# Kernel tuning notes

Hardware: AMD Instinct MI355X
Metric: run time of the kernel (lower is better)

Reference implementation:

```python
import jax, jax.numpy as jnp
import numpy as np

EPS = float(np.finfo(float).eps)
NUM_RFS = 1

def conv3d(x, w):
    # x: [N,C,D,H,W], w: [O,I,kd,kh,kw], VALID, stride 1 (matches F.conv3d defaults)
    return jax.lax.conv_general_dilated(
        x, w, window_strides=(1, 1, 1), padding='VALID',
        dimension_numbers=('NCDHW', 'OIDHW', 'NCDHW'))

def setup_inputs() -> dict:
    key = jax.random.key(0)
    k1, k2, k3, k4 = jax.random.split(key, 4)
    x = jax.random.normal(k1, (1, 1, 3, 394, 394), jnp.float32)
    x_prev = jax.random.normal(k2, (1, 1, 3, 394, 394), jnp.float32)
    # params stored post-permute as [out_ch, in_ch, kt, kh, kw]
    filts_temp = jax.random.normal(k3, (16, 1, 3, 11, 11), jnp.float32)
    filts_notemp = jax.random.normal(k4, (16, 1, 1, 11, 11), jnp.float32)
    return {"x": x, "x_prev": x_prev, "filts_temp": filts_temp, "filts_notemp": filts_notemp}

def reference(x, x_prev, filts_temp, filts_notemp):
    corr_x = NUM_RFS * filts_temp.shape[3]  # kh
    corr_y = NUM_RFS * filts_temp.shape[4]  # kw
    num_filts = filts_temp.shape[0] + filts_notemp.shape[0]

    def feats(v):
        vt = jax.nn.relu(conv3d(v, filts_temp)) / 2           # [1,16,1,H',W'] (T==kt)
        vn = jax.nn.relu(conv3d(v[:, :, -1:, :, :], filts_notemp))  # last frame, [1,16,1,H',W']
        return jnp.concatenate([vt, vn], axis=1)              # [1,32,1,H',W']

    f = feats(x)
    fp = feats(x_prev)
    # channel-wise normalization
    x1 = f / (jnp.sum(f, axis=1, keepdims=True) + EPS)
    x1_prev = fp / (jnp.sum(fp, axis=1, keepdims=True) + EPS)

    y_max, x_max = x1.shape[3], x1.shape[4]
    yc = y_max - 2 * corr_y
    xc = x_max - 2 * corr_x
    # cropped current-frame channels become conv filters: [nf,1,1,yc,xc]
    x1_filts = x1[:, :, :, corr_y:y_max - corr_y, corr_x:x_max - corr_x].reshape(
        num_filts, 1, 1, yc, xc)
    prev = x1_prev.reshape(1, 1, num_filts, y_max, x_max)
    # normalized cross-correlation via conv3d: out [1, nf, nf, 2cy+1, 2cx+1]
    x2 = conv3d(prev, x1_filts)
    x2 = x2.reshape(1, num_filts, num_filts, 2 * corr_y + 1, 2 * corr_x + 1)
    x2 = x2 / ((y_max - 2 * corr_y) * (x_max - 2 * corr_y))  # faithful to original (uses corr_y twice)
    return x1, x2
```

## Files before the change

### kernel.cpp

```cpp
#include <hip/hip_runtime.h>
#include <hip/hip_bf16.h>


typedef unsigned short ushort_t;
typedef unsigned int uint_t;
typedef unsigned char uchar_t;
typedef __attribute__((ext_vector_type(4))) float f32x4;
typedef __attribute__((ext_vector_type(16))) float f32x16;
typedef __attribute__((ext_vector_type(4))) uint_t uint4_t;
typedef __attribute__((ext_vector_type(2))) uint_t uint2_t;
typedef __attribute__((ext_vector_type(8))) int int8v;

#define EPSF 2.2204460492503131e-16f
#define X1_N (32*384*384)
#define X2_N (32*32*23*23)

#define FILTB_ROW_B 12288
#define FILTB_BYTES (372*48*32*8)
#define PREVB_STRIDE 432
#define PREVB_BYTES (32*385*PREVB_STRIDE)
#define ZERO_BYTES ((size_t)FILTB_BYTES + PREVB_BYTES)
#define FT2_ELEMS (16*45*12)

#define YMAX 367
#define NCHUNKS 16
#define INV_AREA (1.0f/131044.0f)

#define SB_COPY_B 432
#define SB_DYB_B  (8*SB_COPY_B)
#define SB_ROW_B  (4*SB_DYB_B)
#define SB_BYTES  (2*2*SB_ROW_B)

#define SA_BYTES  (8*FILTB_ROW_B)
#define SMEM_TOTAL (SA_BYTES + SB_BYTES)

__device__ __forceinline__ uint_t f32_to_e4m3(float f) {
  if (f < 0.015625f)
    return (uint_t)__float2int_rn(f * 512.0f);
  uint_t b = __builtin_bit_cast(uint_t, f);
  int e = (int)(b >> 23) - 127;
  uint_t m = b & 0x7FFFFFu;
  uint_t keep = m >> 20;
  uint_t rest = m & 0xFFFFFu;
  keep += (rest > 0x80000u) || (rest == 0x80000u && (keep & 1u));
  if (keep == 8u) { keep = 0u; e += 1; }
  if (e > 8) return 0x7Eu;
  return (uint_t)(((e + 7) << 3) | keep);
}

__global__ void prep_kernel(const float* __restrict__ ft, const float* __restrict__ fn,
                            float* __restrict__ fT2)
{
  const int e = blockIdx.x * 256 + threadIdx.x;
  if (e < FT2_ELEMS) {
    const int chp = e / 540;
    const int rem = e - chp * 540;
    const int row = rem / 12;
    const int j = rem - row * 12;
    float v = 0.f;
    if (j < 11) {
      if (row < 33)      v = ft[chp * 363 + row * 11 + j];
      else if (row < 44) v = fn[chp * 121 + (row - 33) * 11 + j];
    }
    fT2[e] = v;
  }
}

__global__ __launch_bounds__(128, 4) void feat_kernel(
    const float* __restrict__ xcur, const float* __restrict__ xprev,
    const float* __restrict__ fT2,
    float* __restrict__ out_x1, uchar_t* __restrict__ prevb)
{
  __shared__ float sPx[3 * 18 * 28];
  const int tid = threadIdx.x;
  const int chp = tid & 15;
  const int r = tid >> 4;
  const int j0 = blockIdx.x * 16;
  const int i0 = blockIdx.y * 8;
  const int i = i0 + r;
  const int mode = blockIdx.z;
  const float* __restrict__ xin = mode ? xprev : xcur;

  for (int e = tid; e < 3 * 18 * 26; e += 128) {
    const int t = e / 468;
    const int rem = e - t * 468;
    const int ri = rem / 26;
    const int ci = rem - ri * 26;
    sPx[(t * 18 + ri) * 28 + ci] = xin[((size_t)t * 394 + i0 + ri) * 394 + j0 + ci];
  }
  __syncthreads();

  const float* __restrict__ fbase = fT2 + chp * 540;

  float accT[16], accN[16];
#pragma unroll
  for (int p = 0; p < 16; ++p) { accT[p] = 0.f; accN[p] = 0.f; }

#pragma unroll
  for (int t = 0; t < 3; ++t) {
    for (int a = 0; a < 11; ++a) {
      const float* row = &sPx[(t * 18 + r + a) * 28];
      float wv[26];
#pragma unroll
      for (int k = 0; k < 6; ++k) {
        const f32x4 q = *(const f32x4*)(row + 4 * k);
        wv[4 * k + 0] = q[0]; wv[4 * k + 1] = q[1];
        wv[4 * k + 2] = q[2]; wv[4 * k + 3] = q[3];
      }
      wv[24] = row[24]; wv[25] = row[25];

      const float* fr = fbase + (t * 11 + a) * 12;
      const f32x4 fq0 = *(const f32x4*)(fr);
      const f32x4 fq1 = *(const f32x4*)(fr + 4);
      const f32x4 fq2 = *(const f32x4*)(fr + 8);
      float fv[12];
#pragma unroll
      for (int k = 0; k < 4; ++k) { fv[k] = fq0[k]; fv[4+k] = fq1[k]; fv[8+k] = fq2[k]; }
      float fv2[12];
      if (t == 2) {
        const float* fr2 = fbase + (33 + a) * 12;
        const f32x4 g0 = *(const f32x4*)(fr2);
        const f32x4 g1 = *(const f32x4*)(fr2 + 4);
        const f32x4 g2 = *(const f32x4*)(fr2 + 8);
#pragma unroll
        for (int k = 0; k < 4; ++k) { fv2[k] = g0[k]; fv2[4+k] = g1[k]; fv2[8+k] = g2[k]; }
      }

#pragma unroll
      for (int b = 0; b < 11; ++b) {
        const float fT = fv[b];
#pragma unroll
        for (int p = 0; p < 16; ++p) accT[p] = fmaf(wv[b + p], fT, accT[p]);
        if (t == 2) {
          const float fN = fv2[b];
#pragma unroll
          for (int p = 0; p < 16; ++p) accN[p] = fmaf(wv[b + p], fN, accN[p]);
        }
      }
    }
  }

  float o0[16], o1[16];
#pragma unroll
  for (int p = 0; p < 16; ++p) {
    const float vT = fmaxf(accT[p], 0.f) * 0.5f;
    const float vN = fmaxf(accN[p], 0.f);
    float s = vT + vN;
    s += __shfl_xor(s, 1);  s += __shfl_xor(s, 2);
    s += __shfl_xor(s, 4);  s += __shfl_xor(s, 8);
    const float inv = 1.f / (s + EPSF);
    o0[p] = vT * inv;
    o1[p] = vN * inv;
  }

  if (mode == 0) {
#pragma unroll
    for (int q = 0; q < 4; ++q) {
      f32x4 v0 = {o0[4*q], o0[4*q+1], o0[4*q+2], o0[4*q+3]};
      f32x4 v1 = {o1[4*q], o1[4*q+1], o1[4*q+2], o1[4*q+3]};
      *(f32x4*)(out_x1 + (size_t)chp * 147456 + i * 384 + j0 + 4 * q) = v0;
      *(f32x4*)(out_x1 + (size_t)(chp + 16) * 147456 + i * 384 + j0 + 4 * q) = v1;
    }
  } else {
    uint4_t u0, u1;
#pragma unroll
    for (int q = 0; q < 4; ++q) {
      u0[q] = f32_to_e4m3(o0[4*q]) | (f32_to_e4m3(o0[4*q+1]) << 8) |
              (f32_to_e4m3(o0[4*q+2]) << 16) | (f32_to_e4m3(o0[4*q+3]) << 24);
      u1[q] = f32_to_e4m3(o1[4*q]) | (f32_to_e4m3(o1[4*q+1]) << 8) |
              (f32_to_e4m3(o1[4*q+2]) << 16) | (f32_to_e4m3(o1[4*q+3]) << 24);
    }
    *(uint4_t*)(prevb + ((size_t)chp * 385 + i) * PREVB_STRIDE + j0) = u0;
    *(uint4_t*)(prevb + ((size_t)(chp + 16) * 385 + i) * PREVB_STRIDE + j0) = u1;
  }
}

__global__ __launch_bounds__(256) void pack_kernel(
    const float* __restrict__ x1, uchar_t* __restrict__ filtb)
{
  const int e = blockIdx.x * 256 + threadIdx.x;
  if (e >= 362 * 46 * 32) return;
  const int o = e & 31;
  const int q = e >> 5;
  const int xb = q % 46;
  const int rowr = q / 46 + 5;
  const int i = rowr + 6;
  const int j0 = 11 + xb * 8;
  const float* src = x1 + (size_t)o * 147456 + i * 384 + j0;
  uint_t w0 = 0, w1 = 0;
#pragma unroll
  for (int k = 0; k < 4; ++k) {
    w0 |= f32_to_e4m3((j0 + k     <= 372) ? src[k]     : 0.f) << (8 * k);
    w1 |= f32_to_e4m3((j0 + 4 + k <= 372) ? src[4 + k] : 0.f) << (8 * k);
  }
  uint2_t u = {w0, w1};
  const int off = (xb >> 3) * 2048 + ((xb >> 1) & 1) * 1024 +
                  ((xb >> 2) & 1) * 512 + o * 16 + (xb & 1) * 8;
  *(uint2_t*)(filtb + (size_t)rowr * FILTB_ROW_B + off) = u;
}

__global__ __launch_bounds__(768, 3) void corr_kernel(
    const uchar_t* __restrict__ filtb, const uchar_t* __restrict__ prevb,
    float* __restrict__ x2)
{
  extern __shared__ uchar_t smem[];

  const int tid = threadIdx.x;
  const int lane = tid & 63;
  const int wv = tid >> 6;
  const int cg = (wv >= 6) ? 1 : 0;
  const int w = wv - 6 * cg;
  const int kg = lane >> 5;
  const int nn = lane & 31;

  const int chpair = blockIdx.x / NCHUNKS;
  const int chunk = blockIdx.x % NCHUNKS;
  const int ch = 2 * chpair + cg;
  const int y0 = (chunk * YMAX) / NCHUNKS;
  const int y1 = ((chunk + 1) * YMAX) / NCHUNKS;

  uint_t* const sBg = (uint_t*)(smem + SA_BYTES) + cg * (2 * (SB_ROW_B / 4));

  int boffB[3];
#pragma unroll
  for (int nt = 0; nt < 3; ++nt) {
    const int n = nt * 32 + nn;
    const int dyb = n / 24;
    const int dxr = n - 24 * dyb;
    const int dx = (dxr < 23) ? dxr : 22;
    const int s = dx & 7;
    boffB[nt] = dyb * SB_DYB_B + s * SB_COPY_B + (dx >> 3) * 8 + kg * 32;
  }

  const int tl = tid - cg * 384;
  const bool st_act = (tl < 104);
  const int sdyb = st_act ? (tl / 26) : 0;
  const int sg = tl - 26 * (st_act ? (tl / 26) : 0);
  const uchar_t* srcbase = prevb + ((size_t)(ch * 385 + 6 * sdyb)) * PREVB_STRIDE;
  const int dstoff = sdyb * (SB_DYB_B / 4) + 4 * sg;

  uint_t st0 = 0, st1 = 0, st2 = 0, st3 = 0, st4 = 0, st5 = 0;

  auto load_st = [&](int yy) {
    const uint_t* sw = (const uint_t*)(srcbase + (size_t)yy * PREVB_STRIDE) + 4 * sg;
    const uint4_t lo = *(const uint4_t*)(sw);
    const uint2_t hi = *(const uint2_t*)(sw + 4);
    st0 = lo.x; st1 = lo.y; st2 = lo.z; st3 = lo.w; st4 = hi.x; st5 = hi.y;
  };

  auto write_shift = [&](int buf) {
    uint_t* dst = sBg + buf * (SB_ROW_B / 4) + dstoff;
    const uint_t wd[6] = {st0, st1, st2, st3, st4, st5};
#pragma unroll
    for (int s = 0; s < 8; ++s) {
      const int off = s >> 2;
      const int b = (s & 3) * 8;
      uint4_t v;
      if (b == 0) {
        v = uint4_t{wd[off], wd[off + 1], wd[off + 2], wd[off + 3]};
      } else {
        v = uint4_t{(wd[off]     >> b) | (wd[off + 1] << (32 - b)),
                    (wd[off + 1] >> b) | (wd[off + 2] << (32 - b)),
                    (wd[off + 2] >> b) | (wd[off + 3] << (32 - b)),
                    (wd[off + 3] >> b) | (wd[off + 4] << (32 - b))};
      }
      *(uint4_t*)(dst + s * (SB_COPY_B / 4)) = v;
    }
  };

  f32x16 acc[3];
#pragma unroll
  for (int nt = 0; nt < 3; ++nt)
#pragma unroll
    for (int r = 0; r < 16; ++r) acc[nt][r] = 0.f;

  {
    uint4_t pv[6];
#pragma unroll
    for (int r6 = 0; r6 < 6; ++r6)
      pv[r6] = *(const uint4_t*)(filtb + (size_t)(y0 + r6) * FILTB_ROW_B + tid * 16);
#pragma unroll
    for (int r6 = 0; r6 < 6; ++r6)
      *(uint4_t*)(smem + ((y0 + r6) & 7) * FILTB_ROW_B + tid * 16) = pv[r6];
  }
  if (st_act) {
    load_st(y0);
    write_shift(0);
    if (y0 + 1 < y1) load_st(y0 + 1);
  }

  __syncthreads();

  for (int y = y0; y < y1; ++y) {
    const int pb = (y - y0) & 1;

    const bool a_act = (y + 6 <= y1 + 4);
    uint4_t aval;
    if (a_act)
      aval = *(const uint4_t*)(filtb + (size_t)(y + 6) * FILTB_ROW_B + tid * 16);

    if (st_act && y + 1 < y1) write_shift(pb ^ 1);
    if (st_act && y + 2 < y1) load_st(y + 2);

    const char* sBrd = (const char*)sBg + pb * SB_ROW_B;
    const char* aRow = (const char*)smem +
        ((y + 5 - w) & 7) * FILTB_ROW_B + kg * 512 + nn * 16;

#pragma unroll 1
    for (int kt = 0; kt < 6; ++kt) {
      const char* ap = aRow + (kt << 11);
      const uint4_t a0 = *(const uint4_t*)(ap);
      const uint4_t a1 = *(const uint4_t*)(ap + 1024);
      const int8v Af = {(int)a0.x, (int)a0.y, (int)a0.z, (int)a0.w,
                        (int)a1.x, (int)a1.y, (int)a1.z, (int)a1.w};
#pragma unroll
      for (int nt = 0; nt < 3; ++nt) {
        const char* bp = sBrd + boffB[nt] + (kt << 6);
        const uint2_t b0 = *(const uint2_t*)(bp);
        const uint2_t b1 = *(const uint2_t*)(bp + 8);
        const uint2_t b2 = *(const uint2_t*)(bp + 16);
        const uint2_t b3 = *(const uint2_t*)(bp + 24);
        const int8v Bf = {(int)b0.x, (int)b0.y, (int)b1.x, (int)b1.y,
                          (int)b2.x, (int)b2.y, (int)b3.x, (int)b3.y};
        acc[nt] = __builtin_amdgcn_mfma_scale_f32_32x32x64_f8f6f4(
            Af, Bf, acc[nt], 0, 0,
            0, 0x7F7F7F7F, 0, 0x7F7F7F7F);
      }
    }

    if (a_act)
      *(uint4_t*)(smem + ((y + 6) & 7) * FILTB_ROW_B + tid * 16) = aval;

    __syncthreads();
  }

#pragma unroll
  for (int nt = 0; nt < 3; ++nt) {
    const int n = nt * 32 + nn;
    const int dyb = n / 24;
    const int dxr = n - 24 * dyb;
    if (dxr < 23) {
      const int dy = w + 6 * dyb;
      if (dy <= 22) {
#pragma unroll
        for (int r = 0; r < 16; ++r) {
          const int o = (r & 3) + 8 * (r >> 2) + 4 * kg;
          atomicAdd(&x2[((o * 32 + ch) * 23 + dy) * 23 + dxr],
                    acc[nt][r] * INV_AREA);
        }
      }
    }
  }
}

extern "C" void kernel_launch(void* const* d_in, const int* in_sizes, int n_in,
                              void* d_out, int out_size, void* d_ws, size_t ws_size,
                              hipStream_t stream)
{
  const float* x     = (const float*)d_in[0];
  const float* xprev = (const float*)d_in[1];
  const float* ft    = (const float*)d_in[2];
  const float* fn    = (const float*)d_in[3];
  float* out = (float*)d_out;

  uchar_t* filtb = (uchar_t*)d_ws;
  uchar_t* prevb = filtb + FILTB_BYTES;
  float* fT2 = (float*)(prevb + PREVB_BYTES);

  static bool attr_set = false;
  if (!attr_set) {
    (void)hipFuncSetAttribute((const void*)corr_kernel,
        hipFuncAttributeMaxDynamicSharedMemorySize, SMEM_TOTAL);
    attr_set = true;
  }

  hipMemsetAsync(d_ws, 0, ZERO_BYTES, stream);
  hipMemsetAsync(out + X1_N, 0, (size_t)X2_N * sizeof(float), stream);

  prep_kernel<<<dim3((FT2_ELEMS + 255) / 256), 256, 0, stream>>>(ft, fn, fT2);
  feat_kernel<<<dim3(24, 48, 2), 128, 0, stream>>>(x, xprev, fT2, out, prevb);
  pack_kernel<<<dim3((362 * 46 * 32 + 255) / 256), 256, 0, stream>>>(out, filtb);
  corr_kernel<<<dim3(16 * NCHUNKS), 768, SMEM_TOTAL, stream>>>(
      filtb, prevb, out + X1_N);
}
```

Measured before the change: 276.5 us.

## Software-pipeline MFMA operand loads, pad shared B rows, stage x1 stores via LDS

The correlation kernel's inner loop now prefetches the next A fragment and the next B fragment from shared memory while the current MFMA runs, so LDS latency overlaps matrix work. The per-dy block stride in the shared B buffer gets 16 bytes of padding, presumably to reduce bank conflicts. The feature kernel stages normalized x1 outputs through a shared tile so each thread writes contiguous 16-byte chunks in a coalesced pattern. In exchange there is extra register pressure from the double-buffered operands, more shared memory use, and an added barrier in the feature kernel.

Measured after the change: 278.9 us. Within noise of the previous version (+0.9%).

```diff
diff --git a/kernel.cpp b/kernel.cpp
--- a/kernel.cpp
+++ b/kernel.cpp
@@ -27,7 +27,7 @@
 #define INV_AREA (1.0f/131044.0f)
 
 #define SB_COPY_B 432
-#define SB_DYB_B  (8*SB_COPY_B)
+#define SB_DYB_B  (8*SB_COPY_B + 16)
 #define SB_ROW_B  (4*SB_DYB_B)
 #define SB_BYTES  (2*2*SB_ROW_B)
 
@@ -72,6 +72,7 @@
     float* __restrict__ out_x1, uchar_t* __restrict__ prevb)
 {
   __shared__ float sPx[3 * 18 * 28];
+  __shared__ float sOut[32][9][20];
   const int tid = threadIdx.x;
   const int chp = tid & 15;
   const int r = tid >> 4;
@@ -155,11 +156,20 @@
 
   if (mode == 0) {
 #pragma unroll
-    for (int q = 0; q < 4; ++q) {
-      f32x4 v0 = {o0[4*q], o0[4*q+1], o0[4*q+2], o0[4*q+3]};
-      f32x4 v1 = {o1[4*q], o1[4*q+1], o1[4*q+2], o1[4*q+3]};
-      *(f32x4*)(out_x1 + (size_t)chp * 147456 + i * 384 + j0 + 4 * q) = v0;
-      *(f32x4*)(out_x1 + (size_t)(chp + 16) * 147456 + i * 384 + j0 + 4 * q) = v1;
+    for (int p = 0; p < 16; ++p) {
+      sOut[chp][r][p] = o0[p];
+      sOut[chp + 16][r][p] = o1[p];
+    }
+    __syncthreads();
+#pragma unroll
+    for (int it = 0; it < 8; ++it) {
+      const int idx = it * 128 + tid;
+      const int seg = idx & 3;
+      const int rr = (idx >> 2) & 7;
+      const int chn = idx >> 5;
+      const f32x4 v = {sOut[chn][rr][4 * seg], sOut[chn][rr][4 * seg + 1],
+                       sOut[chn][rr][4 * seg + 2], sOut[chn][rr][4 * seg + 3]};
+      *(f32x4*)(out_x1 + (size_t)chn * 147456 + (i0 + rr) * 384 + j0 + 4 * seg) = v;
     }
   } else {
     uint4_t u0, u1;
@@ -306,26 +316,67 @@
     const char* aRow = (const char*)smem +
         ((y + 5 - w) & 7) * FILTB_ROW_B + kg * 512 + nn * 16;
 
+    int8v Af, Afn, Bf, Bfn;
+    {
+      const uint4_t a0 = *(const uint4_t*)(aRow);
+      const uint4_t a1 = *(const uint4_t*)(aRow + 1024);
+      Af = int8v{(int)a0.x, (int)a0.y, (int)a0.z, (int)a0.w,
+                 (int)a1.x, (int)a1.y, (int)a1.z, (int)a1.w};
+      const char* bp = sBrd + boffB[0];
+      const uint2_t b0 = *(const uint2_t*)(bp);
+      const uint2_t b1 = *(const uint2_t*)(bp + 8);
+      const uint2_t b2 = *(const uint2_t*)(bp + 16);
+      const uint2_t b3 = *(const uint2_t*)(bp + 24);
+      Bf = int8v{(int)b0.x, (int)b0.y, (int)b1.x, (int)b1.y,
+                 (int)b2.x, (int)b2.y, (int)b3.x, (int)b3.y};
+    }
 #pragma unroll 1
     for (int kt = 0; kt < 6; ++kt) {
-      const char* ap = aRow + (kt << 11);
-      const uint4_t a0 = *(const uint4_t*)(ap);
-      const uint4_t a1 = *(const uint4_t*)(ap + 1024);
-      const int8v Af = {(int)a0.x, (int)a0.y, (int)a0.z, (int)a0.w,
-                        (int)a1.x, (int)a1.y, (int)a1.z, (int)a1.w};
-#pragma unroll
-      for (int nt = 0; nt < 3; ++nt) {
-        const char* bp = sBrd + boffB[nt] + (kt << 6);
+      const int ktn = (kt < 5) ? kt + 1 : 5;
+      {
+        const char* ap = aRow + (ktn << 11);
+        const uint4_t a0 = *(const uint4_t*)(ap);
+        const uint4_t a1 = *(const uint4_t*)(ap + 1024);
+        Afn = int8v{(int)a0.x, (int)a0.y, (int)a0.z, (int)a0.w,
+                    (int)a1.x, (int)a1.y, (int)a1.z, (int)a1.w};
+      }
+      {
+        const char* bp = sBrd + boffB[1] + (kt << 6);
         const uint2_t b0 = *(const uint2_t*)(bp);
         const uint2_t b1 = *(const uint2_t*)(bp + 8);
         const uint2_t b2 = *(const uint2_t*)(bp + 16);
         const uint2_t b3 = *(const uint2_t*)(bp + 24);
-        const int8v Bf = {(int)b0.x, (int)b0.y, (int)b1.x, (int)b1.y,
-                          (int)b2.x, (int)b2.y, (int)b3.x, (int)b3.y};
-        acc[nt] = __builtin_amdgcn_mfma_scale_f32_32x32x64_f8f6f4(
-            Af, Bf, acc[nt], 0, 0,
-            0, 0x7F7F7F7F, 0, 0x7F7F7F7F);
-      }
+        Bfn = int8v{(int)b0.x, (int)b0.y, (int)b1.x, (int)b1.y,
+                    (int)b2.x, (int)b2.y, (int)b3.x, (int)b3.y};
+      }
+      acc[0] = __builtin_amdgcn_mfma_scale_f32_32x32x64_f8f6f4(
+          Af, Bf, acc[0], 0, 0, 0, 0x7F7F7F7F, 0, 0x7F7F7F7F);
+      Bf = Bfn;
+      {
+        const char* bp = sBrd + boffB[2] + (kt << 6);
+        const uint2_t b0 = *(const uint2_t*)(bp);
+        const uint2_t b1 = *(const uint2_t*)(bp + 8);
+        const uint2_t b2 = *(const uint2_t*)(bp + 16);
+        const uint2_t b3 = *(const uint2_t*)(bp + 24);
+        Bfn = int8v{(int)b0.x, (int)b0.y, (int)b1.x, (int)b1.y,
+                    (int)b2.x, (int)b2.y, (int)b3.x, (int)b3.y};
+      }
+      acc[1] = __builtin_amdgcn_mfma_scale_f32_32x32x64_f8f6f4(
+          Af, Bf, acc[1], 0, 0, 0, 0x7F7F7F7F, 0, 0x7F7F7F7F);
+      Bf = Bfn;
+      {
+        const char* bp = sBrd + boffB[0] + (ktn << 6);
+        const uint2_t b0 = *(const uint2_t*)(bp);
+        const uint2_t b1 = *(const uint2_t*)(bp + 8);
+        const uint2_t b2 = *(const uint2_t*)(bp + 16);
+        const uint2_t b3 = *(const uint2_t*)(bp + 24);
+        Bfn = int8v{(int)b0.x, (int)b0.y, (int)b1.x, (int)b1.y,
+                    (int)b2.x, (int)b2.y, (int)b3.x, (int)b3.y};
+      }
+      acc[2] = __builtin_amdgcn_mfma_scale_f32_32x32x64_f8f6f4(
+          Af, Bf, acc[2], 0, 0, 0, 0x7F7F7F7F, 0, 0x7F7F7F7F);
+      Bf = Bfn;
+      Af = Afn;
     }
 
     if (a_act)
```

## Split corr K across wave pairs for B-fragment reuse; stage x1 stores via LDS

Applied to the files above, without the earlier changes.

In the correlation kernel, each wave now computes two dy offsets (two accumulator sets) over half of the K range, selected by kh. This lets each B fragment loaded from shared memory feed two MFMAs instead of one. The partial sums from the two K halves are combined through the existing atomicAdd epilogue. The feature kernel now stages x1 outputs in shared memory so that each global store writes contiguous 64-byte row segments per channel. The change doubles accumulator register use, which risks spills at the 768-thread launch bound, and adds a shared buffer and a barrier to the feature kernel.

After: 323.1 us. 16.8% more time.

```diff
diff --git a/kernel.cpp b/kernel.cpp
--- a/kernel.cpp
+++ b/kernel.cpp
@@ -72,6 +72,7 @@
     float* __restrict__ out_x1, uchar_t* __restrict__ prevb)
 {
   __shared__ float sPx[3 * 18 * 28];
+  __shared__ float sOut[32][9][20];
   const int tid = threadIdx.x;
   const int chp = tid & 15;
   const int r = tid >> 4;
@@ -155,11 +156,20 @@
 
   if (mode == 0) {
 #pragma unroll
-    for (int q = 0; q < 4; ++q) {
-      f32x4 v0 = {o0[4*q], o0[4*q+1], o0[4*q+2], o0[4*q+3]};
-      f32x4 v1 = {o1[4*q], o1[4*q+1], o1[4*q+2], o1[4*q+3]};
-      *(f32x4*)(out_x1 + (size_t)chp * 147456 + i * 384 + j0 + 4 * q) = v0;
-      *(f32x4*)(out_x1 + (size_t)(chp + 16) * 147456 + i * 384 + j0 + 4 * q) = v1;
+    for (int p = 0; p < 16; ++p) {
+      sOut[chp][r][p] = o0[p];
+      sOut[chp + 16][r][p] = o1[p];
+    }
+    __syncthreads();
+#pragma unroll
+    for (int it = 0; it < 8; ++it) {
+      const int idx = it * 128 + tid;
+      const int seg = idx & 3;
+      const int rr = (idx >> 2) & 7;
+      const int chn = idx >> 5;
+      const f32x4 v = {sOut[chn][rr][4 * seg], sOut[chn][rr][4 * seg + 1],
+                       sOut[chn][rr][4 * seg + 2], sOut[chn][rr][4 * seg + 3]};
+      *(f32x4*)(out_x1 + (size_t)chn * 147456 + (i0 + rr) * 384 + j0 + 4 * seg) = v;
     }
   } else {
     uint4_t u0, u1;
@@ -209,7 +219,9 @@
   const int lane = tid & 63;
   const int wv = tid >> 6;
   const int cg = (wv >= 6) ? 1 : 0;
-  const int w = wv - 6 * cg;
+  const int gw = wv - 6 * cg;
+  const int p = gw >> 1;
+  const int kh = gw & 1;
   const int kg = lane >> 5;
   const int nn = lane & 31;
 
@@ -229,7 +241,8 @@
     const int dxr = n - 24 * dyb;
     const int dx = (dxr < 23) ? dxr : 22;
     const int s = dx & 7;
-    boffB[nt] = dyb * SB_DYB_B + s * SB_COPY_B + (dx >> 3) * 8 + kg * 32;
+    boffB[nt] = dyb * SB_DYB_B + s * SB_COPY_B + (dx >> 3) * 8 + kg * 32
+              + kh * 192;
   }
 
   const int tl = tid - cg * 384;
@@ -268,11 +281,13 @@
     }
   };
 
-  f32x16 acc[3];
-#pragma unroll
-  for (int nt = 0; nt < 3; ++nt)
-#pragma unroll
-    for (int r = 0; r < 16; ++r) acc[nt][r] = 0.f;
+  f32x16 acc[2][3];
+#pragma unroll
+  for (int m = 0; m < 2; ++m)
+#pragma unroll
+    for (int nt = 0; nt < 3; ++nt)
+#pragma unroll
+      for (int r = 0; r < 16; ++r) acc[m][nt][r] = 0.f;
 
   {
     uint4_t pv[6];
@@ -303,16 +318,21 @@
     if (st_act && y + 2 < y1) load_st(y + 2);
 
     const char* sBrd = (const char*)sBg + pb * SB_ROW_B;
-    const char* aRow = (const char*)smem +
-        ((y + 5 - w) & 7) * FILTB_ROW_B + kg * 512 + nn * 16;
+    const char* aRow0 = (const char*)smem +
+        ((y + 5 - 2 * p) & 7) * FILTB_ROW_B + kh * 6144 + kg * 512 + nn * 16;
+    const char* aRow1 = (const char*)smem +
+        ((y + 4 - 2 * p) & 7) * FILTB_ROW_B + kh * 6144 + kg * 512 + nn * 16;
 
 #pragma unroll 1
-    for (int kt = 0; kt < 6; ++kt) {
-      const char* ap = aRow + (kt << 11);
-      const uint4_t a0 = *(const uint4_t*)(ap);
-      const uint4_t a1 = *(const uint4_t*)(ap + 1024);
-      const int8v Af = {(int)a0.x, (int)a0.y, (int)a0.z, (int)a0.w,
-                        (int)a1.x, (int)a1.y, (int)a1.z, (int)a1.w};
+    for (int kt = 0; kt < 3; ++kt) {
+      const uint4_t a00 = *(const uint4_t*)(aRow0 + (kt << 11));
+      const uint4_t a01 = *(const uint4_t*)(aRow0 + (kt << 11) + 1024);
+      const int8v Af0 = {(int)a00.x, (int)a00.y, (int)a00.z, (int)a00.w,
+                         (int)a01.x, (int)a01.y, (int)a01.z, (int)a01.w};
+      const uint4_t a10 = *(const uint4_t*)(aRow1 + (kt << 11));
+      const uint4_t a11 = *(const uint4_t*)(aRow1 + (kt << 11) + 1024);
+      const int8v Af1 = {(int)a10.x, (int)a10.y, (int)a10.z, (int)a10.w,
+                         (int)a11.x, (int)a11.y, (int)a11.z, (int)a11.w};
 #pragma unroll
       for (int nt = 0; nt < 3; ++nt) {
         const char* bp = sBrd + boffB[nt] + (kt << 6);
@@ -322,9 +342,10 @@
         const uint2_t b3 = *(const uint2_t*)(bp + 24);
         const int8v Bf = {(int)b0.x, (int)b0.y, (int)b1.x, (int)b1.y,
                           (int)b2.x, (int)b2.y, (int)b3.x, (int)b3.y};
-        acc[nt] = __builtin_amdgcn_mfma_scale_f32_32x32x64_f8f6f4(
-            Af, Bf, acc[nt], 0, 0,
-            0, 0x7F7F7F7F, 0, 0x7F7F7F7F);
+        acc[0][nt] = __builtin_amdgcn_mfma_scale_f32_32x32x64_f8f6f4(
+            Af0, Bf, acc[0][nt], 0, 0, 0, 0x7F7F7F7F, 0, 0x7F7F7F7F);
+        acc[1][nt] = __builtin_amdgcn_mfma_scale_f32_32x32x64_f8f6f4(
+            Af1, Bf, acc[1][nt], 0, 0, 0, 0x7F7F7F7F, 0, 0x7F7F7F7F);
       }
     }
 
@@ -335,18 +356,22 @@
   }
 
 #pragma unroll
-  for (int nt = 0; nt < 3; ++nt) {
-    const int n = nt * 32 + nn;
-    const int dyb = n / 24;
-    const int dxr = n - 24 * dyb;
-    if (dxr < 23) {
-      const int dy = w + 6 * dyb;
-      if (dy <= 22) {
-#pragma unroll
-        for (int r = 0; r < 16; ++r) {
-          const int o = (r & 3) + 8 * (r >> 2) + 4 * kg;
-          atomicAdd(&x2[((o * 32 + ch) * 23 + dy) * 23 + dxr],
-                    acc[nt][r] * INV_AREA);
+  for (int m = 0; m < 2; ++m) {
+    const int dya = 2 * p + m;
+#pragma unroll
+    for (int nt = 0; nt < 3; ++nt) {
+      const int n = nt * 32 + nn;
+      const int dyb = n / 24;
+      const int dxr = n - 24 * dyb;
+      if (dxr < 23) {
+        const int dy = dya + 6 * dyb;
+        if (dy <= 22) {
+#pragma unroll
+          for (int r = 0; r < 16; ++r) {
+            const int o = (r & 3) + 8 * (r >> 2) + 4 * kg;
+            atomicAdd(&x2[((o * 32 + ch) * 23 + dy) * 23 + dxr],
+                      acc[m][nt][r] * INV_AREA);
+          }
         }
       }
     }
```

## Warp-specialize corr kernel with producer waves and stage x1 stores through LDS

Applied to the files above, without the earlier changes.

The correlation kernel gains four producer waves (block size 768→1024) that copy filter rows and shifted prev rows into shared memory while twelve compute waves run only the MFMA loop, replacing the earlier scheme where compute threads also did the staging. The aim is to take global-load latency and shift work off the MFMA waves. Separately, the feature kernel now stages its normalized outputs in shared memory so each x1 row segment is written to global memory with coalesced vector stores. This costs extra LDS use and a barrier, and the larger block may reduce the number of blocks that fit per CU.

After: 276.3 us. About the same (-0.1%).

```diff
diff --git a/kernel.cpp b/kernel.cpp
--- a/kernel.cpp
+++ b/kernel.cpp
@@ -72,6 +72,7 @@
     float* __restrict__ out_x1, uchar_t* __restrict__ prevb)
 {
   __shared__ float sPx[3 * 18 * 28];
+  __shared__ float sOut[32][9][20];
   const int tid = threadIdx.x;
   const int chp = tid & 15;
   const int r = tid >> 4;
@@ -155,11 +156,20 @@
 
   if (mode == 0) {
 #pragma unroll
-    for (int q = 0; q < 4; ++q) {
-      f32x4 v0 = {o0[4*q], o0[4*q+1], o0[4*q+2], o0[4*q+3]};
-      f32x4 v1 = {o1[4*q], o1[4*q+1], o1[4*q+2], o1[4*q+3]};
-      *(f32x4*)(out_x1 + (size_t)chp * 147456 + i * 384 + j0 + 4 * q) = v0;
-      *(f32x4*)(out_x1 + (size_t)(chp + 16) * 147456 + i * 384 + j0 + 4 * q) = v1;
+    for (int p = 0; p < 16; ++p) {
+      sOut[chp][r][p] = o0[p];
+      sOut[chp + 16][r][p] = o1[p];
+    }
+    __syncthreads();
+#pragma unroll
+    for (int it = 0; it < 8; ++it) {
+      const int idx = it * 128 + tid;
+      const int seg = idx & 3;
+      const int rr = (idx >> 2) & 7;
+      const int chn = idx >> 5;
+      const f32x4 v = {sOut[chn][rr][4 * seg], sOut[chn][rr][4 * seg + 1],
+                       sOut[chn][rr][4 * seg + 2], sOut[chn][rr][4 * seg + 3]};
+      *(f32x4*)(out_x1 + (size_t)chn * 147456 + (i0 + rr) * 384 + j0 + 4 * seg) = v;
     }
   } else {
     uint4_t u0, u1;
@@ -199,7 +209,7 @@
   *(uint2_t*)(filtb + (size_t)rowr * FILTB_ROW_B + off) = u;
 }
 
-__global__ __launch_bounds__(768, 3) void corr_kernel(
+__global__ __launch_bounds__(1024, 4) void corr_kernel(
     const uchar_t* __restrict__ filtb, const uchar_t* __restrict__ prevb,
     float* __restrict__ x2)
 {
@@ -208,18 +218,20 @@
   const int tid = threadIdx.x;
   const int lane = tid & 63;
   const int wv = tid >> 6;
-  const int cg = (wv >= 6) ? 1 : 0;
-  const int w = wv - 6 * cg;
+  const bool is_comp = (wv < 12);
+  const int pw = wv - 12;
+  const int cgu = is_comp ? ((wv >= 6) ? 1 : 0) : (pw >> 1);
+  const int w = is_comp ? (wv - 6 * ((wv >= 6) ? 1 : 0)) : 0;
   const int kg = lane >> 5;
   const int nn = lane & 31;
 
   const int chpair = blockIdx.x / NCHUNKS;
   const int chunk = blockIdx.x % NCHUNKS;
-  const int ch = 2 * chpair + cg;
+  const int ch = 2 * chpair + cgu;
   const int y0 = (chunk * YMAX) / NCHUNKS;
   const int y1 = ((chunk + 1) * YMAX) / NCHUNKS;
 
-  uint_t* const sBg = (uint_t*)(smem + SA_BYTES) + cg * (2 * (SB_ROW_B / 4));
+  uint_t* const sBg = (uint_t*)(smem + SA_BYTES) + cgu * (2 * (SB_ROW_B / 4));
 
   int boffB[3];
 #pragma unroll
@@ -232,25 +244,19 @@
     boffB[nt] = dyb * SB_DYB_B + s * SB_COPY_B + (dx >> 3) * 8 + kg * 32;
   }
 
-  const int tl = tid - cg * 384;
-  const bool st_act = (tl < 104);
-  const int sdyb = st_act ? (tl / 26) : 0;
-  const int sg = tl - 26 * (st_act ? (tl / 26) : 0);
+  const int tl = is_comp ? 0 : ((pw & 1) * 64 + lane);
+  const bool b_act = (!is_comp) && (tl < 104);
+  const int sdyb = b_act ? (tl / 26) : 0;
+  const int sg = tl - 26 * (b_act ? (tl / 26) : 0);
   const uchar_t* srcbase = prevb + ((size_t)(ch * 385 + 6 * sdyb)) * PREVB_STRIDE;
   const int dstoff = sdyb * (SB_DYB_B / 4) + 4 * sg;
 
-  uint_t st0 = 0, st1 = 0, st2 = 0, st3 = 0, st4 = 0, st5 = 0;
-
-  auto load_st = [&](int yy) {
+  auto stage_B = [&](int yy, int buf) {
     const uint_t* sw = (const uint_t*)(srcbase + (size_t)yy * PREVB_STRIDE) + 4 * sg;
     const uint4_t lo = *(const uint4_t*)(sw);
     const uint2_t hi = *(const uint2_t*)(sw + 4);
-    st0 = lo.x; st1 = lo.y; st2 = lo.z; st3 = lo.w; st4 = hi.x; st5 = hi.y;
-  };
-
-  auto write_shift = [&](int buf) {
+    const uint_t wd[6] = {lo.x, lo.y, lo.z, lo.w, hi.x, hi.y};
     uint_t* dst = sBg + buf * (SB_ROW_B / 4) + dstoff;
-    const uint_t wd[6] = {st0, st1, st2, st3, st4, st5};
 #pragma unroll
     for (int s = 0; s < 8; ++s) {
       const int off = s >> 2;
@@ -268,85 +274,84 @@
     }
   };
 
+  const int ptid = is_comp ? 0 : (pw * 64 + lane);
+  auto stage_A = [&](int row, int slot) {
+    const uchar_t* src = filtb + (size_t)row * FILTB_ROW_B + ptid * 48;
+    uchar_t* dst = smem + (size_t)slot * FILTB_ROW_B + ptid * 48;
+    const uint4_t v0 = *(const uint4_t*)(src);
+    const uint4_t v1 = *(const uint4_t*)(src + 16);
+    const uint4_t v2 = *(const uint4_t*)(src + 32);
+    *(uint4_t*)(dst) = v0;
+    *(uint4_t*)(dst + 16) = v1;
+    *(uint4_t*)(dst + 32) = v2;
+  };
+
   f32x16 acc[3];
 #pragma unroll
   for (int nt = 0; nt < 3; ++nt)
 #pragma unroll
     for (int r = 0; r < 16; ++r) acc[nt][r] = 0.f;
 
-  {
-    uint4_t pv[6];
+  if (!is_comp) {
 #pragma unroll
     for (int r6 = 0; r6 < 6; ++r6)
-      pv[r6] = *(const uint4_t*)(filtb + (size_t)(y0 + r6) * FILTB_ROW_B + tid * 16);
-#pragma unroll
-    for (int r6 = 0; r6 < 6; ++r6)
-      *(uint4_t*)(smem + ((y0 + r6) & 7) * FILTB_ROW_B + tid * 16) = pv[r6];
-  }
-  if (st_act) {
-    load_st(y0);
-    write_shift(0);
-    if (y0 + 1 < y1) load_st(y0 + 1);
-  }
-
+      stage_A(y0 + r6, (y0 + r6) & 7);
+    if (b_act) stage_B(y0, 0);
+  }
   __syncthreads();
 
   for (int y = y0; y < y1; ++y) {
     const int pb = (y - y0) & 1;
 
-    const bool a_act = (y + 6 <= y1 + 4);
-    uint4_t aval;
-    if (a_act)
-      aval = *(const uint4_t*)(filtb + (size_t)(y + 6) * FILTB_ROW_B + tid * 16);
-
-    if (st_act && y + 1 < y1) write_shift(pb ^ 1);
-    if (st_act && y + 2 < y1) load_st(y + 2);
-
-    const char* sBrd = (const char*)sBg + pb * SB_ROW_B;
-    const char* aRow = (const char*)smem +
-        ((y + 5 - w) & 7) * FILTB_ROW_B + kg * 512 + nn * 16;
+    if (is_comp) {
+      const char* sBrd = (const char*)sBg + pb * SB_ROW_B;
+      const char* aRow = (const char*)smem +
+          ((y + 5 - w) & 7) * FILTB_ROW_B + kg * 512 + nn * 16;
 
 #pragma unroll 1
-    for (int kt = 0; kt < 6; ++kt) {
-      const char* ap = aRow + (kt << 11);
-      const uint4_t a0 = *(const uint4_t*)(ap);
-      const uint4_t a1 = *(const uint4_t*)(ap + 1024);
-      const int8v Af = {(int)a0.x, (int)a0.y, (int)a0.z, (int)a0.w,
-                        (int)a1.x, (int)a1.y, (int)a1.z, (int)a1.w};
-#pragma unroll
-      for (int nt = 0; nt < 3; ++nt) {
-        const char* bp = sBrd + boffB[nt] + (kt << 6);
-        const uint2_t b0 = *(const uint2_t*)(bp);
-        const uint2_t b1 = *(const uint2_t*)(bp + 8);
-        const uint2_t b2 = *(const uint2_t*)(bp + 16);
-        const uint2_t b3 = *(const uint2_t*)(bp + 24);
-        const int8v Bf = {(int)b0.x, (int)b0.y, (int)b1.x, (int)b1.y,
-                          (int)b2.x, (int)b2.y, (int)b3.x, (int)b3.y};
-        acc[nt] = __builtin_amdgcn_mfma_scale_f32_32x32x64_f8f6f4(
-            Af, Bf, acc[nt], 0, 0,
-            0, 0x7F7F7F7F, 0, 0x7F7F7F7F);
-      }
-    }
-
-    if (a_act)
-      *(uint4_t*)(smem + ((y + 6) & 7) * FILTB_ROW_B + tid * 16) = aval;
+      for (int kt = 0; kt < 6; ++kt) {
+        const char* ap = aRow + (kt << 11);
+        const uint4_t a0 = *(const uint4_t*)(ap);
+        const uint4_t a1 = *(const uint4_t*)(ap + 1024);
+        const int8v Af = {(int)a0.x, (int)a0.y, (int)a0.z, (int)a0.w,
+                          (int)a1.x, (int)a1.y, (int)a1.z, (int)a1.w};
+#pragma unroll
+        for (int nt = 0; nt < 3; ++nt) {
+          const char* bp = sBrd + boffB[nt] + (kt << 6);
+          const uint2_t b0 = *(const uint2_t*)(bp);
+          const uint2_t b1 = *(const uint2_t*)(bp + 8);
+          const uint2_t b2 = *(const uint2_t*)(bp + 16);
+          const uint2_t b3 = *(const uint2_t*)(bp + 24);
+          const int8v Bf = {(int)b0.x, (int)b0.y, (int)b1.x, (int)b1.y,
+                            (int)b2.x, (int)b2.y, (int)b3.x, (int)b3.y};
+          acc[nt] = __builtin_amdgcn_mfma_scale_f32_32x32x64_f8f6f4(
+              Af, Bf, acc[nt], 0, 0,
+              0, 0x7F7F7F7F, 0, 0x7F7F7F7F);
+        }
+      }
+    } else {
+      if (b_act && y + 1 < y1) stage_B(y + 1, pb ^ 1);
+      if (y + 6 <= y1 + 4) stage_A(y + 6, (y + 6) & 7);
+    }
 
     __syncthreads();
   }
 
-#pragma unroll
-  for (int nt = 0; nt < 3; ++nt) {
-    const int n = nt * 32 + nn;
-    const int dyb = n / 24;
-    const int dxr = n - 24 * dyb;
-    if (dxr < 23) {
-      const int dy = w + 6 * dyb;
-      if (dy <= 22) {
-#pragma unroll
-        for (int r = 0; r < 16; ++r) {
-          const int o = (r & 3) + 8 * (r >> 2) + 4 * kg;
-          atomicAdd(&x2[((o * 32 + ch) * 23 + dy) * 23 + dxr],
-                    acc[nt][r] * INV_AREA);
+  if (is_comp) {
+#pragma unroll
+    for (int nt = 0; nt < 3; ++nt) {
+      const int n = nt * 32 + nn;
+      const int dyb = n / 24;
+      const int dxr = n - 24 * dyb;
+      if (dxr < 23) {
+        const int dy = w + 6 * dyb;
+        if (dy <= 22) {
+#pragma unroll
+          for (int r = 0; r < 16; ++r) {
+            const int o = (r & 3) + 8 * (r >> 2) + 4 * kg;
+            atomicAdd(&x2[((o * 32 + ch) * 23 + dy) * 23 + dxr],
+                      acc[nt][r] * INV_AREA);
+          }
         }
       }
     }
@@ -380,6 +385,6 @@
   prep_kernel<<<dim3((FT2_ELEMS + 255) / 256), 256, 0, stream>>>(ft, fn, fT2);
   feat_kernel<<<dim3(24, 48, 2), 128, 0, stream>>>(x, xprev, fT2, out, prevb);
   pack_kernel<<<dim3((362 * 46 * 32 + 255) / 256), 256, 0, stream>>>(out, filtb);
-  corr_kernel<<<dim3(16 * NCHUNKS), 768, SMEM_TOTAL, stream>>>(
+  corr_kernel<<<dim3(16 * NCHUNKS), 1024, SMEM_TOTAL, stream>>>(
       filtb, prevb, out + X1_N);
 }
```
